# Kernel optimization log

Hardware: AMD Instinct MI355X
Metric: run time of the kernel (lower is better)

## Reference

```python
import jax, jax.numpy as jnp
import numpy as np

FP8_E4M3_MAX = 448.0  # torch.finfo(torch.float8_e4m3fn).max
TOKENS, D_IN, D_OUT = 8192, 4096, 4096


def setup_inputs() -> dict:
    key = jax.random.key(0)
    kx, kw, kb = jax.random.split(key, 3)
    x = jax.random.normal(kx, (TOKENS, D_IN), dtype=jnp.float32)
    # frozen bf16-like master weight, quantized to fp8 with per-tensor scale (as in __init__)
    w = jax.random.normal(kw, (D_OUT, D_IN), dtype=jnp.float32) * 0.02
    amax = jnp.abs(w).max()
    weight_scale = jnp.maximum(amax / FP8_E4M3_MAX, 1e-12).reshape(1)
    weight_fp8 = (w / weight_scale).astype(jnp.float8_e4m3fn)
    bias = jax.random.normal(kb, (D_OUT,), dtype=jnp.float32) * 0.01
    return {"x": x, "weight_fp8": weight_fp8, "weight_scale": weight_scale, "bias": bias}


def reference(x, weight_fp8, weight_scale, bias):
    # dequantize fp8 weight to activation dtype, scalar per-tensor scale
    w = weight_fp8.astype(x.dtype) * weight_scale.astype(x.dtype)  # [D_OUT, D_IN]
    return x @ w.T + bias  # [TOKENS, D_OUT]
```

## Files before the change

kernel.cpp:

```cpp
#include <hip/hip_runtime.h>


#define TILE 128
#define BKK  64
#define BK32 32
#define BM256 256
#define BN256 256

typedef __attribute__((ext_vector_type(8))) __bf16 bfrag8;
typedef __attribute__((ext_vector_type(4))) float  f32x4;
typedef __attribute__((ext_vector_type(8))) short  s8v;

#define GLOBAL_AS(p) ((const __attribute__((address_space(1))) void*)(p))
#define LDS_AS(p)    ((__attribute__((address_space(3))) void*)(p))

__device__ inline unsigned short f2bf(float f) {
    union { float f; unsigned u; } v; v.f = f;
    unsigned r = v.u + 0x7FFFu + ((v.u >> 16) & 1u);
    return (unsigned short)(r >> 16);
}
__device__ inline float bf2f(unsigned short u) {
    union { unsigned u; float f; } v; v.u = ((unsigned)u) << 16;
    return v.f;
}

__device__ inline int detect_w_f32(const void* w) {
    const unsigned short* u = (const unsigned short*)w;
    unsigned nz = 0;
#pragma unroll
    for (int i = 0; i < 64; ++i) nz |= u[2 * i];
    return nz == 0 ? 1 : 0;
}

__global__ void FP8FL_cvt_x(const float* __restrict__ x, short* __restrict__ xb, long n) {
    long i = ((long)blockIdx.x * blockDim.x + threadIdx.x) * 8;
    if (i >= n) return;
    float4 a = *(const float4*)(x + i);
    float4 b = *(const float4*)(x + i + 4);
    s8v r;
    r[0] = (short)f2bf(a.x); r[1] = (short)f2bf(a.y);
    r[2] = (short)f2bf(a.z); r[3] = (short)f2bf(a.w);
    r[4] = (short)f2bf(b.x); r[5] = (short)f2bf(b.y);
    r[6] = (short)f2bf(b.z); r[7] = (short)f2bf(b.w);
    *(s8v*)(xb + i) = r;
}

__global__ void FP8FL_cvt_w(const void* __restrict__ w, short* __restrict__ wb,
                            const float* __restrict__ scale_p, long n) {
    __shared__ int sdt;
    if (threadIdx.x == 0) sdt = detect_w_f32(w);
    __syncthreads();
    long i = ((long)blockIdx.x * blockDim.x + threadIdx.x) * 8;
    if (i >= n) return;
    const float s = scale_p[0];
    s8v r;
    if (sdt) {
        const float* wf = (const float*)w;
        float4 a = *(const float4*)(wf + i);
        float4 b = *(const float4*)(wf + i + 4);
        r[0] = (short)f2bf(a.x * s); r[1] = (short)f2bf(a.y * s);
        r[2] = (short)f2bf(a.z * s); r[3] = (short)f2bf(a.w * s);
        r[4] = (short)f2bf(b.x * s); r[5] = (short)f2bf(b.y * s);
        r[6] = (short)f2bf(b.z * s); r[7] = (short)f2bf(b.w * s);
    } else {
        const unsigned short* wu = (const unsigned short*)w;
        s8v v = *(const s8v*)(wu + i);
#pragma unroll
        for (int j = 0; j < 8; ++j)
            r[j] = (short)f2bf(bf2f((unsigned short)v[j]) * s);
    }
    *(s8v*)(wb + i) = r;
}

__device__ inline void stage_tile3(const short* __restrict__ A, const short* __restrict__ B,
                                   long row0, long col0, int K, int kc,
                                   char* __restrict__ lds, int s, int wid, int lane) {
    char* Asl = lds + s * 32768;
    char* Bsl = Asl + 16384;
#pragma unroll
    for (int i = 0; i < 2; ++i) {
        int pc = i * 512 + wid * 64 + lane;
        int r  = pc >> 2;
        int j  = (pc & 3) ^ ((r >> 1) & 3);
        const short* ga = A + (size_t)(row0 + r) * K + kc + j * 8;
        const short* gb = B + (size_t)(col0 + r) * K + kc + j * 8;
        char* da = Asl + (i * 512 + wid * 64) * 16;
        char* db = Bsl + (i * 512 + wid * 64) * 16;
        __builtin_amdgcn_global_load_lds(GLOBAL_AS(ga), LDS_AS(da), 16, 0, 0);
        __builtin_amdgcn_global_load_lds(GLOBAL_AS(gb), LDS_AS(db), 16, 0, 0);
    }
}

__global__ __launch_bounds__(512, 2)
void FP8FL_gemm256(const short* __restrict__ A, const short* __restrict__ B,
                   const float* __restrict__ bias, float* __restrict__ C,
                   int M, int N, int K) {
    __shared__ char lds[3 * 32768];

    const int tid  = threadIdx.x;
    const int lane = tid & 63;
    const int wid  = tid >> 6;

    const int nwg = gridDim.x;
    const int bid = blockIdx.x;
    const int wg  = (nwg % 8 == 0) ? (bid % 8) * (nwg / 8) + (bid / 8) : bid;

    const int tiles_n = N / BN256;
    const long row0 = (long)(wg / tiles_n) * BM256;
    const long col0 = (long)(wg % tiles_n) * BN256;

    const int wm = wid >> 2, wn = wid & 3;
    const int rl = lane & 15, g = lane >> 4;

    f32x4 acc[8][4];
#pragma unroll
    for (int m = 0; m < 8; ++m)
#pragma unroll
        for (int n = 0; n < 4; ++n) acc[m][n] = (f32x4){0.f, 0.f, 0.f, 0.f};

    const int NT = K / BK32;

    stage_tile3(A, B, row0, col0, K, 0,    lds, 0, wid, lane);
    stage_tile3(A, B, row0, col0, K, BK32, lds, 1, wid, lane);
    asm volatile("s_waitcnt vmcnt(4)" ::: "memory");
    __builtin_amdgcn_s_barrier();
    __builtin_amdgcn_sched_barrier(0);

    int scur = 0, snxt = 2;
    for (int t = 0; t < NT; ++t) {
        if (t + 2 < NT)
            stage_tile3(A, B, row0, col0, K, (t + 2) * BK32, lds, snxt, wid, lane);

        const char* Asl = lds + scur * 32768;
        const char* Bsl = Asl + 16384;
        bfrag8 af[8], bf[4];
#pragma unroll
        for (int m = 0; m < 8; ++m) {
            int r  = wm * 128 + m * 16 + rl;
            int sl = g ^ ((r >> 1) & 3);
            af[m] = *(const bfrag8*)(Asl + (r * 4 + sl) * 16);
        }
#pragma unroll
        for (int n = 0; n < 4; ++n) {
            int r  = wn * 64 + n * 16 + rl;
            int sl = g ^ ((r >> 1) & 3);
            bf[n] = *(const bfrag8*)(Bsl + (r * 4 + sl) * 16);
        }

        __builtin_amdgcn_s_setprio(1);
#pragma unroll
        for (int m = 0; m < 8; ++m)
#pragma unroll
            for (int n = 0; n < 4; ++n)
                acc[m][n] = __builtin_amdgcn_mfma_f32_16x16x32_bf16(af[m], bf[n], acc[m][n], 0, 0, 0);
        __builtin_amdgcn_s_setprio(0);

        if (t + 2 < NT) asm volatile("s_waitcnt vmcnt(4)" ::: "memory");
        else            asm volatile("s_waitcnt vmcnt(0)" ::: "memory");
        __builtin_amdgcn_s_barrier();
        __builtin_amdgcn_sched_barrier(0);

        scur = (scur == 2) ? 0 : scur + 1;
        snxt = (snxt == 2) ? 0 : snxt + 1;
    }

    float bv[4];
#pragma unroll
    for (int n = 0; n < 4; ++n) bv[n] = bias[col0 + wn * 64 + n * 16 + rl];
#pragma unroll
    for (int m = 0; m < 8; ++m) {
#pragma unroll
        for (int jj = 0; jj < 4; ++jj) {
            long r = row0 + wm * 128 + m * 16 + g * 4 + jj;
            float* cp = C + r * (long)N + col0 + wn * 64 + rl;
#pragma unroll
            for (int n = 0; n < 4; ++n) cp[n * 16] = acc[m][n][jj] + bv[n];
        }
    }
}

__global__ void FP8FL_gemm(const short* __restrict__ A, const short* __restrict__ B,
                           const float* __restrict__ bias, float* __restrict__ C,
                           int M, int N, int K) {
    __shared__ short As[TILE * BKK];
    __shared__ short Bs[TILE * BKK];

    const int tid  = threadIdx.x;
    const int lane = tid & 63;
    const int wid  = tid >> 6;

    const int nwg = gridDim.x;
    const int bid = blockIdx.x;
    const int wg  = (nwg % 8 == 0) ? (bid % 8) * (nwg / 8) + (bid / 8) : bid;

    const int tiles_n = N / TILE;
    const long row0 = (long)(wg / tiles_n) * TILE;
    const long col0 = (long)(wg % tiles_n) * TILE;

    const int wm = wid >> 1, wn = wid & 1;

    f32x4 acc[4][4];
#pragma unroll
    for (int i = 0; i < 4; ++i)
#pragma unroll
        for (int j = 0; j < 4; ++j) acc[i][j] = (f32x4){0.f, 0.f, 0.f, 0.f};

    const int rl = lane & 15;
    const int g  = lane >> 4;

    for (int k0 = 0; k0 < K; k0 += BKK) {
        __syncthreads();
#pragma unroll
        for (int i = 0; i < 4; ++i) {
            int c  = i * 256 + tid;
            int r  = c >> 3;
            int ls = c & 7;
            const short* ga = A + ((size_t)(row0 + r) * K + k0 + ls * 8);
            const short* gb = B + ((size_t)(col0 + r) * K + k0 + ls * 8);
            int ldsoff = (i * 256 + wid * 64) * 16;
            __builtin_amdgcn_global_load_lds(GLOBAL_AS(ga), LDS_AS((char*)As + ldsoff), 16, 0, 0);
            __builtin_amdgcn_global_load_lds(GLOBAL_AS(gb), LDS_AS((char*)Bs + ldsoff), 16, 0, 0);
        }
        __syncthreads();

#pragma unroll
        for (int kk = 0; kk < 2; ++kk) {
            bfrag8 af[4], bfr[4];
            const int lsk = kk * 4 + g;
#pragma unroll
            for (int m = 0; m < 4; ++m) {
                int r  = wm * 64 + m * 16 + rl;
                af[m] = *(const bfrag8*)&As[r * 64 + lsk * 8];
            }
#pragma unroll
            for (int n = 0; n < 4; ++n) {
                int r  = wn * 64 + n * 16 + rl;
                bfr[n] = *(const bfrag8*)&Bs[r * 64 + lsk * 8];
            }
#pragma unroll
            for (int m = 0; m < 4; ++m)
#pragma unroll
                for (int n = 0; n < 4; ++n)
                    acc[m][n] = __builtin_amdgcn_mfma_f32_16x16x32_bf16(af[m], bfr[n], acc[m][n], 0, 0, 0);
        }
    }

    float bv[4];
#pragma unroll
    for (int n = 0; n < 4; ++n) bv[n] = bias[col0 + wn * 64 + n * 16 + rl];
#pragma unroll
    for (int m = 0; m < 4; ++m) {
#pragma unroll
        for (int j = 0; j < 4; ++j) {
            long r = row0 + wm * 64 + m * 16 + g * 4 + j;
            float* cp = C + r * (long)N + col0 + wn * 64 + rl;
#pragma unroll
            for (int n = 0; n < 4; ++n) cp[n * 16] = acc[m][n][j] + bv[n];
        }
    }
}

__global__ void FP8FL_gemm_fused(const float* __restrict__ X, const void* __restrict__ W,
                                 const float* __restrict__ scale_p,
                                 const float* __restrict__ bias, float* __restrict__ C,
                                 int M, int N, int K) {
    __shared__ short As[TILE * BKK];
    __shared__ short Bs[TILE * BKK];
    __shared__ int sdt;

    const int tid  = threadIdx.x;
    const int lane = tid & 63;
    const int wid  = tid >> 6;

    if (tid == 0) sdt = detect_w_f32(W);
    __syncthreads();
    const int wdt = sdt;
    const float s = scale_p[0];

    const int nwg = gridDim.x;
    const int bid = blockIdx.x;
    const int wg  = (nwg % 8 == 0) ? (bid % 8) * (nwg / 8) + (bid / 8) : bid;

    const int tiles_n = N / TILE;
    const long row0 = (long)(wg / tiles_n) * TILE;
    const long col0 = (long)(wg % tiles_n) * TILE;

    const int wm = wid >> 1, wn = wid & 1;

    f32x4 acc[4][4];
#pragma unroll
    for (int i = 0; i < 4; ++i)
#pragma unroll
        for (int j = 0; j < 4; ++j) acc[i][j] = (f32x4){0.f, 0.f, 0.f, 0.f};

    const int rl = lane & 15;
    const int g  = lane >> 4;

    for (int k0 = 0; k0 < K; k0 += BKK) {
        s8v va[4], vb[4];
#pragma unroll
        for (int i = 0; i < 4; ++i) {
            int c  = i * 256 + tid;
            int r  = c >> 3;
            int ls = c & 7;
            {
                const float* xp = X + ((size_t)(row0 + r) * K + k0 + ls * 8);
                float4 a = *(const float4*)xp;
                float4 b = *(const float4*)(xp + 4);
                s8v t;
                t[0] = (short)f2bf(a.x); t[1] = (short)f2bf(a.y);
                t[2] = (short)f2bf(a.z); t[3] = (short)f2bf(a.w);
                t[4] = (short)f2bf(b.x); t[5] = (short)f2bf(b.y);
                t[6] = (short)f2bf(b.z); t[7] = (short)f2bf(b.w);
                va[i] = t;
            }
            {
                size_t off = (size_t)(col0 + r) * K + k0 + ls * 8;
                s8v t;
                if (wdt) {
                    const float* wp = (const float*)W + off;
                    float4 a = *(const float4*)wp;
                    float4 b = *(const float4*)(wp + 4);
                    t[0] = (short)f2bf(a.x * s); t[1] = (short)f2bf(a.y * s);
                    t[2] = (short)f2bf(a.z * s); t[3] = (short)f2bf(a.w * s);
                    t[4] = (short)f2bf(b.x * s); t[5] = (short)f2bf(b.y * s);
                    t[6] = (short)f2bf(b.z * s); t[7] = (short)f2bf(b.w * s);
                } else {
                    const unsigned short* wp = (const unsigned short*)W + off;
                    s8v v = *(const s8v*)wp;
#pragma unroll
                    for (int j = 0; j < 8; ++j)
                        t[j] = (short)f2bf(bf2f((unsigned short)v[j]) * s);
                }
                vb[i] = t;
            }
        }
        __syncthreads();
#pragma unroll
        for (int i = 0; i < 4; ++i) {
            int c = i * 256 + tid;
            *(s8v*)((char*)As + (size_t)c * 16) = va[i];
            *(s8v*)((char*)Bs + (size_t)c * 16) = vb[i];
        }
        __syncthreads();

#pragma unroll
        for (int kk = 0; kk < 2; ++kk) {
            bfrag8 af[4], bfr[4];
            const int lsk = kk * 4 + g;
#pragma unroll
            for (int m = 0; m < 4; ++m) {
                int r  = wm * 64 + m * 16 + rl;
                af[m] = *(const bfrag8*)&As[r * 64 + lsk * 8];
            }
#pragma unroll
            for (int n = 0; n < 4; ++n) {
                int r  = wn * 64 + n * 16 + rl;
                bfr[n] = *(const bfrag8*)&Bs[r * 64 + lsk * 8];
            }
#pragma unroll
            for (int m = 0; m < 4; ++m)
#pragma unroll
                for (int n = 0; n < 4; ++n)
                    acc[m][n] = __builtin_amdgcn_mfma_f32_16x16x32_bf16(af[m], bfr[n], acc[m][n], 0, 0, 0);
        }
    }

    float bv[4];
#pragma unroll
    for (int n = 0; n < 4; ++n) bv[n] = bias[col0 + wn * 64 + n * 16 + rl];
#pragma unroll
    for (int m = 0; m < 4; ++m) {
#pragma unroll
        for (int j = 0; j < 4; ++j) {
            long r = row0 + wm * 64 + m * 16 + g * 4 + j;
            float* cp = C + r * (long)N + col0 + wn * 64 + rl;
#pragma unroll
            for (int n = 0; n < 4; ++n) cp[n * 16] = acc[m][n][j] + bv[n];
        }
    }
}

__global__ void FP8FL_naive(const float* __restrict__ x, const void* __restrict__ w,
                            const float* __restrict__ scale_p, const float* __restrict__ bias,
                            float* __restrict__ out, int M, int N, int K) {
    __shared__ int sdt;
    if (threadIdx.x == 0) sdt = detect_w_f32(w);
    __syncthreads();
    long o = (long)blockIdx.x * blockDim.x + threadIdx.x;
    if (o >= (long)M * N) return;
    int m = (int)(o / N), n = (int)(o % N);
    const float* xr = x + (size_t)m * K;
    float acc = 0.f;
    if (sdt) {
        const float* wr = (const float*)w + (size_t)n * K;
        for (int k = 0; k < K; ++k) acc += xr[k] * wr[k];
    } else {
        const unsigned short* wr = (const unsigned short*)w + (size_t)n * K;
        for (int k = 0; k < K; ++k) acc += xr[k] * bf2f(wr[k]);
    }
    out[o] = acc * scale_p[0] + bias[n];
}

extern "C" void kernel_launch(void* const* d_in, const int* in_sizes, int n_in,
                              void* d_out, int out_size, void* d_ws, size_t ws_size,
                              hipStream_t stream) {
    const float* x     = (const float*)d_in[0];
    const void*  w     = d_in[1];
    const float* scale = (const float*)d_in[2];
    const float* bias  = (const float*)d_in[3];
    float*       out   = (float*)d_out;

    const int N = in_sizes[3];
    const int K = in_sizes[1] / N;
    const int M = in_sizes[0] / K;

    const size_t need = (size_t)M * K * 2 + (size_t)N * K * 2;
    const bool ws_ok   = ws_size >= need;
    const bool dims256 = (M % BM256 == 0) && (N % BN256 == 0) && (K % BKK == 0) && (K / BK32 >= 4);
    const bool dims128 = (M % TILE == 0) && (N % TILE == 0) && (K % BKK == 0);

    if (ws_ok && (dims256 || dims128)) {
        short* xb = (short*)d_ws;
        short* wb = (short*)((char*)d_ws + (size_t)M * K * 2);
        long nx = (long)M * K;
        long nw = (long)N * K;
        FP8FL_cvt_x<<<(int)((nx / 8 + 255) / 256), 256, 0, stream>>>(x, xb, nx);
        FP8FL_cvt_w<<<(int)((nw / 8 + 255) / 256), 256, 0, stream>>>(w, wb, scale, nw);
        if (dims256) {
            int grid = (M / BM256) * (N / BN256);
            FP8FL_gemm256<<<grid, 512, 0, stream>>>(xb, wb, bias, out, M, N, K);
        } else {
            int grid = (M / TILE) * (N / TILE);
            FP8FL_gemm<<<grid, 256, 0, stream>>>(xb, wb, bias, out, M, N, K);
        }
    } else if (dims128) {
        int grid = (M / TILE) * (N / TILE);
        FP8FL_gemm_fused<<<grid, 256, 0, stream>>>(x, w, scale, bias, out, M, N, K);
    } else {
        long total = (long)M * N;
        FP8FL_naive<<<(int)((total + 255) / 256), 256, 0, stream>>>(x, w, scale, bias, out, M, N, K);
    }
}
```

Baseline: 291.5 us.

## Restructure 256x256 GEMM into four-quadrant ping-pong schedule with BK=64 double buffering

Replaces the triple-buffered BK=32 main loop with a double-buffered BK=64 loop. Each wave now computes four 64x32 sub-blocks (2x2 halves), and A/B half-tile loads are interleaved with MFMA phases behind barriers, in the style of HipKittens 8-wave ping-pong. The goal is to hide global-to-LDS latency behind compute and to cut LDS fragment reads by reusing A and B fragments across quadrants. It raises LDS use to 128KB and adds many barriers per iteration, which may limit occupancy and add synchronisation overhead.

New measurement: 289.1 us. About the same (-0.8%).

```diff
diff --git a/kernel.cpp b/kernel.cpp
--- a/kernel.cpp
+++ b/kernel.cpp
@@ -3,7 +3,6 @@
 
 #define TILE 128
 #define BKK  64
-#define BK32 32
 #define BM256 256
 #define BN256 256
 
@@ -72,30 +71,67 @@
     *(s8v*)(wb + i) = r;
 }
 
-__device__ inline void stage_tile3(const short* __restrict__ A, const short* __restrict__ B,
-                                   long row0, long col0, int K, int kc,
-                                   char* __restrict__ lds, int s, int wid, int lane) {
-    char* Asl = lds + s * 32768;
-    char* Bsl = Asl + 16384;
-#pragma unroll
-    for (int i = 0; i < 2; ++i) {
-        int pc = i * 512 + wid * 64 + lane;
-        int r  = pc >> 2;
-        int j  = (pc & 3) ^ ((r >> 1) & 3);
-        const short* ga = A + (size_t)(row0 + r) * K + kc + j * 8;
-        const short* gb = B + (size_t)(col0 + r) * K + kc + j * 8;
-        char* da = Asl + (i * 512 + wid * 64) * 16;
-        char* db = Bsl + (i * 512 + wid * 64) * 16;
-        __builtin_amdgcn_global_load_lds(GLOBAL_AS(ga), LDS_AS(da), 16, 0, 0);
-        __builtin_amdgcn_global_load_lds(GLOBAL_AS(gb), LDS_AS(db), 16, 0, 0);
-    }
-}
+#define STG(P, base0, hrow, kc, dst)                                          \
+    {                                                                         \
+        _Pragma("unroll")                                                     \
+        for (int i_ = 0; i_ < 2; ++i_) {                                      \
+            int pc_ = i_ * 512 + tid;                                         \
+            int r_  = pc_ >> 3;                                               \
+            int j_  = (pc_ & 7) ^ (r_ & 7);                                   \
+            const short* gp_ = (P) + (size_t)((base0) + (hrow) + r_) * K + (kc) + j_ * 8; \
+            char* dp_ = (dst) + (i_ * 512 + wid * 64) * 16;                   \
+            __builtin_amdgcn_global_load_lds(GLOBAL_AS(gp_), LDS_AS(dp_), 16, 0, 0); \
+        }                                                                     \
+    }
+
+#define RD_A8(dst, half)                                                      \
+    {                                                                         \
+        _Pragma("unroll")                                                     \
+        for (int mf_ = 0; mf_ < 4; ++mf_)                                     \
+            _Pragma("unroll")                                                 \
+            for (int kk_ = 0; kk_ < 2; ++kk_) {                               \
+                int r_  = wm * 64 + mf_ * 16 + rl;                            \
+                int sl_ = (kk_ * 4 + g) ^ (r_ & 7);                           \
+                dst[mf_ * 2 + kk_] = *(const bfrag8*)((half) + (r_ * 8 + sl_) * 16); \
+            }                                                                 \
+    }
+
+#define RD_B4(dst, half)                                                      \
+    {                                                                         \
+        _Pragma("unroll")                                                     \
+        for (int nf_ = 0; nf_ < 2; ++nf_)                                     \
+            _Pragma("unroll")                                                 \
+            for (int kk_ = 0; kk_ < 2; ++kk_) {                               \
+                int r_  = wn * 32 + nf_ * 16 + rl;                            \
+                int sl_ = (kk_ * 4 + g) ^ (r_ & 7);                           \
+                dst[nf_ * 2 + kk_] = *(const bfrag8*)((half) + (r_ * 8 + sl_) * 16); \
+            }                                                                 \
+    }
+
+#define MM16(mh, nh, FAa, FBb)                                                \
+    {                                                                         \
+        __builtin_amdgcn_s_setprio(1);                                        \
+        _Pragma("unroll")                                                     \
+        for (int mf_ = 0; mf_ < 4; ++mf_)                                     \
+            _Pragma("unroll")                                                 \
+            for (int nf_ = 0; nf_ < 2; ++nf_)                                 \
+                _Pragma("unroll")                                             \
+                for (int kk_ = 0; kk_ < 2; ++kk_)                             \
+                    acc[mh][nh][mf_][nf_] = __builtin_amdgcn_mfma_f32_16x16x32_bf16( \
+                        FAa[mf_ * 2 + kk_], FBb[nf_ * 2 + kk_],               \
+                        acc[mh][nh][mf_][nf_], 0, 0, 0);                      \
+        __builtin_amdgcn_s_setprio(0);                                        \
+    }
+
+#define LGKM0_FENCE                                                           \
+    asm volatile("s_waitcnt lgkmcnt(0)" ::: "memory");                        \
+    __builtin_amdgcn_sched_barrier(0);
 
 __global__ __launch_bounds__(512, 2)
 void FP8FL_gemm256(const short* __restrict__ A, const short* __restrict__ B,
                    const float* __restrict__ bias, float* __restrict__ C,
                    int M, int N, int K) {
-    __shared__ char lds[3 * 32768];
+    __shared__ char lds[131072];
 
     const int tid  = threadIdx.x;
     const int lane = tid & 63;
@@ -112,71 +148,88 @@
     const int wm = wid >> 2, wn = wid & 3;
     const int rl = lane & 15, g = lane >> 4;
 
-    f32x4 acc[8][4];
-#pragma unroll
-    for (int m = 0; m < 8; ++m)
-#pragma unroll
-        for (int n = 0; n < 4; ++n) acc[m][n] = (f32x4){0.f, 0.f, 0.f, 0.f};
-
-    const int NT = K / BK32;
-
-    stage_tile3(A, B, row0, col0, K, 0,    lds, 0, wid, lane);
-    stage_tile3(A, B, row0, col0, K, BK32, lds, 1, wid, lane);
+    f32x4 acc[2][2][4][2];
+#pragma unroll
+    for (int a0 = 0; a0 < 2; ++a0)
+#pragma unroll
+        for (int a1 = 0; a1 < 2; ++a1)
+#pragma unroll
+            for (int a2 = 0; a2 < 4; ++a2)
+#pragma unroll
+                for (int a3 = 0; a3 < 2; ++a3)
+                    acc[a0][a1][a2][a3] = (f32x4){0.f, 0.f, 0.f, 0.f};
+
+    const int NT = K / BKK;
+
+    {
+        char* b0 = lds;
+        STG(A, row0, 0,   0, b0 + 0);
+        STG(B, col0, 0,   0, b0 + 32768);
+        STG(A, row0, 128, 0, b0 + 16384);
+        STG(B, col0, 128, 0, b0 + 49152);
+    }
     asm volatile("s_waitcnt vmcnt(4)" ::: "memory");
     __builtin_amdgcn_s_barrier();
-    __builtin_amdgcn_sched_barrier(0);
-
-    int scur = 0, snxt = 2;
+
+    bfrag8 FA[8], FB0[4], FB1[4];
+
     for (int t = 0; t < NT; ++t) {
-        if (t + 2 < NT)
-            stage_tile3(A, B, row0, col0, K, (t + 2) * BK32, lds, snxt, wid, lane);
-
-        const char* Asl = lds + scur * 32768;
-        const char* Bsl = Asl + 16384;
-        bfrag8 af[8], bf[4];
-#pragma unroll
-        for (int m = 0; m < 8; ++m) {
-            int r  = wm * 128 + m * 16 + rl;
-            int sl = g ^ ((r >> 1) & 3);
-            af[m] = *(const bfrag8*)(Asl + (r * 4 + sl) * 16);
-        }
-#pragma unroll
-        for (int n = 0; n < 4; ++n) {
-            int r  = wn * 64 + n * 16 + rl;
-            int sl = g ^ ((r >> 1) & 3);
-            bf[n] = *(const bfrag8*)(Bsl + (r * 4 + sl) * 16);
-        }
-
-        __builtin_amdgcn_s_setprio(1);
-#pragma unroll
-        for (int m = 0; m < 8; ++m)
-#pragma unroll
-            for (int n = 0; n < 4; ++n)
-                acc[m][n] = __builtin_amdgcn_mfma_f32_16x16x32_bf16(af[m], bf[n], acc[m][n], 0, 0, 0);
-        __builtin_amdgcn_s_setprio(0);
-
-        if (t + 2 < NT) asm volatile("s_waitcnt vmcnt(4)" ::: "memory");
-        else            asm volatile("s_waitcnt vmcnt(0)" ::: "memory");
-        __builtin_amdgcn_s_barrier();
-        __builtin_amdgcn_sched_barrier(0);
-
-        scur = (scur == 2) ? 0 : scur + 1;
-        snxt = (snxt == 2) ? 0 : snxt + 1;
-    }
-
-    float bv[4];
-#pragma unroll
-    for (int n = 0; n < 4; ++n) bv[n] = bias[col0 + wn * 64 + n * 16 + rl];
-#pragma unroll
-    for (int m = 0; m < 8; ++m) {
-#pragma unroll
-        for (int jj = 0; jj < 4; ++jj) {
-            long r = row0 + wm * 128 + m * 16 + g * 4 + jj;
-            float* cp = C + r * (long)N + col0 + wn * 64 + rl;
-#pragma unroll
-            for (int n = 0; n < 4; ++n) cp[n * 16] = acc[m][n][jj] + bv[n];
-        }
-    }
+        char* cur = lds + (t & 1) * 65536;
+        char* nxt = lds + ((t + 1) & 1) * 65536;
+        const int kc1 = (t + 1) * BKK;
+        const bool pf = (t + 1 < NT);
+
+        RD_A8(FA, cur + 0);
+        RD_B4(FB0, cur + 32768);
+        if (pf) STG(A, row0, 0, kc1, nxt + 0);
+        __builtin_amdgcn_s_barrier();
+        LGKM0_FENCE
+        MM16(0, 0, FA, FB0);
+        if (pf) asm volatile("s_waitcnt vmcnt(2)" ::: "memory");
+        else    asm volatile("s_waitcnt vmcnt(0)" ::: "memory");
+        __builtin_amdgcn_s_barrier();
+
+        RD_B4(FB1, cur + 49152);
+        if (pf) STG(B, col0, 0, kc1, nxt + 32768);
+        __builtin_amdgcn_s_barrier();
+        LGKM0_FENCE
+        MM16(0, 1, FA, FB1);
+        __builtin_amdgcn_s_barrier();
+
+        RD_A8(FA, cur + 16384);
+        if (pf) STG(A, row0, 128, kc1, nxt + 16384);
+        __builtin_amdgcn_s_barrier();
+        LGKM0_FENCE
+        MM16(1, 1, FA, FB1);
+        __builtin_amdgcn_s_barrier();
+
+        if (pf) STG(B, col0, 128, kc1, nxt + 49152);
+        __builtin_amdgcn_s_barrier();
+        MM16(1, 0, FA, FB0);
+        if (pf) asm volatile("s_waitcnt vmcnt(4)" ::: "memory");
+        __builtin_amdgcn_s_barrier();
+    }
+
+    float bv[2][2];
+#pragma unroll
+    for (int nh = 0; nh < 2; ++nh)
+#pragma unroll
+        for (int nf = 0; nf < 2; ++nf)
+            bv[nh][nf] = bias[col0 + nh * 128 + wn * 32 + nf * 16 + rl];
+#pragma unroll
+    for (int mh = 0; mh < 2; ++mh)
+#pragma unroll
+        for (int mf = 0; mf < 4; ++mf)
+#pragma unroll
+            for (int jj = 0; jj < 4; ++jj) {
+                long r = row0 + mh * 128 + wm * 64 + mf * 16 + g * 4 + jj;
+                float* cp = C + r * (long)N + col0 + wn * 32 + rl;
+#pragma unroll
+                for (int nh = 0; nh < 2; ++nh)
+#pragma unroll
+                    for (int nf = 0; nf < 2; ++nf)
+                        cp[nh * 128 + nf * 16] = acc[mh][nh][mf][nf][jj] + bv[nh][nf];
+            }
 }
 
 __global__ void FP8FL_gemm(const short* __restrict__ A, const short* __restrict__ B,
@@ -417,7 +470,7 @@
 
     const size_t need = (size_t)M * K * 2 + (size_t)N * K * 2;
     const bool ws_ok   = ws_size >= need;
-    const bool dims256 = (M % BM256 == 0) && (N % BN256 == 0) && (K % BKK == 0) && (K / BK32 >= 4);
+    const bool dims256 = (M % BM256 == 0) && (N % BN256 == 0) && (K % BKK == 0) && (K / BKK >= 2);
     const bool dims128 = (M % TILE == 0) && (N % TILE == 0) && (K % BKK == 0);
 
     if (ws_ok && (dims256 || dims128)) {
```
